# Performance work log

Hardware: AMD Instinct MI355X
Metric: run time of the kernel (lower is better)

## Reference

```python
import jax, jax.numpy as jnp
import numpy as np

HEADS = 8
GROUPS = 8
EPS = 1e-5

def setup_inputs() -> dict:
    key = jax.random.key(0)
    ks = jax.random.split(key, 12)
    B, C, S = 2, 256, 16
    x = jax.random.normal(ks[0], (B, C, S, S, S), dtype=jnp.float32)
    std = 1.0 / np.sqrt(C)
    def lin(k):
        kw, kb = jax.random.split(k)
        W = jax.random.uniform(kw, (C, C), jnp.float32, -std, std)
        b = jax.random.uniform(kb, (C,), jnp.float32, -std, std)
        return W, b
    Wq, bq = lin(ks[1])
    Wk, bk = lin(ks[2])
    Wv, bv = lin(ks[3])
    Wo, bo = lin(ks[4])
    gamma = jnp.ones((C,), jnp.float32)
    beta = jnp.zeros((C,), jnp.float32)
    return {"x": x, "gamma": gamma, "beta": beta, "Wq": Wq, "bq": bq,
            "Wk": Wk, "bk": bk, "Wv": Wv, "bv": bv, "Wo": Wo, "bo": bo}

def _group_norm(x, gamma, beta):
    B, C = x.shape[0], x.shape[1]
    xg = x.reshape(B, GROUPS, -1)  # [B, G, (C/G)*D*H*W]
    mu = xg.mean(axis=-1, keepdims=True)
    var = xg.var(axis=-1, keepdims=True)
    xg = (xg - mu) * jax.lax.rsqrt(var + EPS)
    xn = xg.reshape(x.shape)
    return xn * gamma[None, :, None, None, None] + beta[None, :, None, None, None]

def _conv1x1(x, W, b):
    # 1x1x1 Conv3d == channel-mixing linear: [B,C,D,H,W] x [O,C]
    return jnp.einsum('bcdhw,oc->bodhw', x, W) + b[None, :, None, None, None]

def reference(x, gamma, beta, Wq, bq, Wk, bk, Wv, bv, Wo, bo):
    B, C, D, H, W = x.shape
    hd = C // HEADS
    N = D * H * W
    xn = _group_norm(x, gamma, beta)
    Q = _conv1x1(xn, Wq, bq).reshape(B, HEADS, hd, N)
    K = _conv1x1(xn, Wk, bk).reshape(B, HEADS, hd, N)
    V = _conv1x1(xn, Wv, bv).reshape(B, HEADS, hd, N)
    scale = jnp.sqrt(jnp.asarray(hd, x.dtype))
    attn = jnp.einsum('bhdn,bhdm->bhnm', Q, K) / scale
    attn = jax.nn.softmax(attn, axis=-1)
    out = jnp.einsum('bhnm,bhdm->bhdn', attn, V).reshape(B, C, D, H, W)
    out = _conv1x1(out, Wo, bo)
    return x + out
```

## Files before the change

### kernel.cpp

```cpp
#include <hip/hip_runtime.h>

typedef unsigned short us;
typedef unsigned int uns;
typedef __attribute__((ext_vector_type(8))) short short8;
typedef __attribute__((ext_vector_type(4))) float floatx4;

__device__ __forceinline__ us f2b(float f) {
    union { float f; unsigned u; } x; x.f = f;
    unsigned r = x.u + 0x7fffu + ((x.u >> 16) & 1u);
    return (us)(r >> 16);
}
__device__ __forceinline__ uns fbits(float f) {
    union { float f; unsigned u; } x; x.f = f; return x.u;
}
__device__ __forceinline__ uns pk2(float hi, float lo) {
    return __builtin_amdgcn_perm(fbits(hi) + 0x8000u, fbits(lo) + 0x8000u, 0x07060302u);
}
__device__ __forceinline__ uns pk2t(float hi, float lo) {
    return __builtin_amdgcn_perm(fbits(hi), fbits(lo), 0x07060302u);
}
__device__ __forceinline__ float ex2(float x) {
    return __builtin_amdgcn_exp2f(x);
}

#define C_DIM 256
#define N_DIM 4096
#define CN (C_DIM * N_DIM)
#define CSC (0.17677669529663687f * 1.4426950408889634f)

__global__ __launch_bounds__(256) void k_part_prep(
        const float* __restrict__ x, float* __restrict__ part,
        const float* __restrict__ Wq, const float* __restrict__ Wk,
        const float* __restrict__ Wv, const float* __restrict__ Wo,
        const float* __restrict__ bq, const float* __restrict__ bk,
        const float* __restrict__ bv, const float* __restrict__ bo,
        us* __restrict__ Wb, float* __restrict__ bst) {
    const int t = threadIdx.x;
    if (blockIdx.y == 16) {
        const int xb = blockIdx.x;
#pragma unroll
        for (int e = 0; e < 4; ++e) {
            int id = e * 16384 + xb * 256 + t;
            Wb[id]          = f2b(Wq[id] * CSC);
            Wb[65536 + id]  = f2b(Wk[id]);
            Wb[131072 + id] = f2b(Wv[id]);
            Wb[196608 + id] = f2b(Wo[id]);
        }
        if (xb == 0) {
            bst[t]       = bq[t] * CSC;
            bst[256 + t] = bk[t];
            bst[512 + t] = bv[t];
            bst[768 + t] = bo[t];
        }
        return;
    }
    const int bg = blockIdx.y, sl = blockIdx.x;
    const float* base = x + (size_t)bg * 131072 + (size_t)sl * 2048 + t * 8;
    float4 a = *(const float4*)base;
    float4 b = *(const float4*)(base + 4);
    float s  = a.x + a.y + a.z + a.w + b.x + b.y + b.z + b.w;
    float ss = a.x*a.x + a.y*a.y + a.z*a.z + a.w*a.w
             + b.x*b.x + b.y*b.y + b.z*b.z + b.w*b.w;
    __shared__ float r1[256], r2[256];
    r1[t] = s; r2[t] = ss;
    __syncthreads();
    for (int off = 128; off > 0; off >>= 1) {
        if (t < off) { r1[t] += r1[t + off]; r2[t] += r2[t + off]; }
        __syncthreads();
    }
    if (t == 0) {
        part[(bg * 64 + sl) * 2]     = r1[0];
        part[(bg * 64 + sl) * 2 + 1] = r2[0];
    }
}

__global__ __launch_bounds__(256) void k_gn_normT(const float* __restrict__ x,
                                                  const float* __restrict__ gamma,
                                                  const float* __restrict__ beta,
                                                  const float* __restrict__ part,
                                                  us* __restrict__ XT) {
    const int t = threadIdx.x, g = blockIdx.y, z = blockIdx.z;
    const int bg = z * 8 + g;
    __shared__ float scs[32], offs[32], mv[2];
    if (t < 64) {
        float s  = part[(bg * 64 + t) * 2];
        float ss = part[(bg * 64 + t) * 2 + 1];
#pragma unroll
        for (int off = 1; off < 64; off <<= 1) {
            s  += __shfl_xor(s, off, 64);
            ss += __shfl_xor(ss, off, 64);
        }
        if (t == 0) {
            const float inv = 1.f / 131072.f;
            float mean = s * inv;
            float var  = ss * inv - mean * mean;
            mv[0] = mean; mv[1] = rsqrtf(var + 1e-5f);
        }
    }
    __syncthreads();
    if (t < 32) {
        float sc = mv[1] * gamma[g * 32 + t];
        scs[t]  = sc;
        offs[t] = beta[g * 32 + t] - mv[0] * sc;
    }
    __syncthreads();
    const int n = blockIdx.x * 256 + t;
    const float* xp = x + ((size_t)z * 256 + g * 32) * N_DIM + n;
    us* op = XT + ((size_t)z * N_DIM + n) * 256 + g * 32;
#pragma unroll
    for (int c8 = 0; c8 < 4; ++c8) {
        short8 o;
#pragma unroll
        for (int i = 0; i < 8; ++i) {
            int c = c8 * 8 + i;
            float v = xp[(size_t)c * N_DIM];
            o[i] = (short)f2b(v * scs[c] + offs[c]);
        }
        *(short8*)(op + c8 * 8) = o;
    }
}

__global__ __launch_bounds__(256) void k_qkv(const us* __restrict__ W,
                                             const float* __restrict__ bias,
                                             const us* __restrict__ XT,
                                             us* __restrict__ QT,
                                             us* __restrict__ KTg,
                                             us* __restrict__ Vb) {
    const int t = threadIdx.x;
    const int n0 = blockIdx.x * 64, m0 = blockIdx.y * 64, z = blockIdx.z;
    const int l = t & 63, w = t >> 6, l15 = l & 15, quad = l >> 4;
    const int wm = m0 + (w >> 1) * 32, wn = n0 + (w & 1) * 32;
    const us* Ap = W + (size_t)(wm + l15) * 256 + quad * 8;
    const us* Bp = XT + ((size_t)z * N_DIM + wn + l15) * 256 + quad * 8;

    floatx4 acc[2][2] = {};
#pragma unroll
    for (int k0 = 0; k0 < 256; k0 += 32) {
        short8 a0 = *(const short8*)(Ap + k0);
        short8 a1 = *(const short8*)(Ap + k0 + 16 * 256);
        short8 b0 = *(const short8*)(Bp + k0);
        short8 b1 = *(const short8*)(Bp + k0 + 16 * 256);
        acc[0][0] = __builtin_amdgcn_mfma_f32_16x16x32_bf16(a0, b0, acc[0][0], 0, 0, 0);
        acc[0][1] = __builtin_amdgcn_mfma_f32_16x16x32_bf16(a0, b1, acc[0][1], 0, 0, 0);
        acc[1][0] = __builtin_amdgcn_mfma_f32_16x16x32_bf16(a1, b0, acc[1][0], 0, 0, 0);
        acc[1][1] = __builtin_amdgcn_mfma_f32_16x16x32_bf16(a1, b1, acc[1][1], 0, 0, 0);
    }

    if (blockIdx.y < 8) {
        us* Dst = (blockIdx.y < 4) ? QT : KTg;
        const int h = (wm >> 5) & 7, bh = z * 8 + h;
#pragma unroll
        for (int mt = 0; mt < 2; ++mt) {
            const int d0 = mt * 16 + quad * 4;
            float b0v = bias[wm + mt * 16 + quad * 4 + 0];
            float b1v = bias[wm + mt * 16 + quad * 4 + 1];
            float b2v = bias[wm + mt * 16 + quad * 4 + 2];
            float b3v = bias[wm + mt * 16 + quad * 4 + 3];
#pragma unroll
            for (int nt = 0; nt < 2; ++nt) {
                int col = wn + nt * 16 + l15;
                uint2 pw;
                pw.x = pk2(acc[mt][nt][1] + b1v, acc[mt][nt][0] + b0v);
                pw.y = pk2(acc[mt][nt][3] + b3v, acc[mt][nt][2] + b2v);
                *(uint2*)(Dst + ((size_t)bh * N_DIM + col) * 32 + d0) = pw;
            }
        }
    } else {
#pragma unroll
        for (int mt = 0; mt < 2; ++mt)
#pragma unroll
            for (int nt = 0; nt < 2; ++nt)
#pragma unroll
                for (int r = 0; r < 4; ++r) {
                    int row = wm + mt * 16 + quad * 4 + r;
                    int col = wn + nt * 16 + l15;
                    Vb[((size_t)z * 256 + (row - 512)) * N_DIM + col] =
                        f2b(acc[mt][nt][r] + bias[row]);
                }
    }
}

__global__ __launch_bounds__(256, 2) void k_attn(const us* __restrict__ QT,
                                                 const us* __restrict__ KTg,
                                                 const us* __restrict__ Vb,
                                                 us* __restrict__ AOT) {
    __shared__ __attribute__((aligned(16))) us Kb[2][64 * 32];
    __shared__ __attribute__((aligned(16))) us Vl[2][32 * 64];
    __shared__ __attribute__((aligned(16))) us Pb[4][2][16 * 104];
    const int t = threadIdx.x;
    const int l = t & 63, w = t >> 6, l15 = l & 15, quad = l >> 4;
    const int bh = blockIdx.y, z = bh >> 3, h = bh & 7;
    const us* KTp = KTg + (size_t)bh * N_DIM * 32;
    const us* Vp  = Vb  + ((size_t)z * 256 + h * 32) * N_DIM;
    const int q0 = blockIdx.x * 128 + w * 32;

    short8 bq[2];
#pragma unroll
    for (int tl = 0; tl < 2; ++tl)
        bq[tl] = *(const short8*)(QT + ((size_t)bh * N_DIM + q0 + tl * 16 + l15) * 32 + quad * 8);
    short8 ones;
#pragma unroll
    for (int j = 0; j < 8; ++j) ones[j] = (short)0x3F80;

    floatx4 o1[2] = {}, o2[2] = {}, o3[2] = {};

    const int krow = w * 16 + (l >> 2), kslot = l & 3;
    const int kxs  = kslot ^ ((l >> 3) & 3);
    const us* kgs  = KTp + (size_t)krow * 32 + kslot * 8;
    us*       kds  = &Kb[0][0] + krow * 32 + kxs * 8;
    const int vrow = w * 8 + (l >> 3), vslot = l & 7;
    const int vxs  = vslot ^ ((l >> 3) & 7);
    const us* vgs  = Vp + (size_t)vrow * N_DIM + vslot * 8;
    us*       vds  = &Vl[0][0] + vrow * 64 + vxs * 8;

    const us* kfr = &Kb[0][0] + l15 * 32 + (quad ^ ((l15 >> 1) & 3)) * 8;
    const int vo1 = ( quad      ^ (l15 & 7)) * 8;
    const int vo2 = ((quad ^ 4) ^ (l15 & 7)) * 8;
    const us* vf1 = &Vl[0][0] +  l15       * 64 + vo1;
    const us* vf2 = &Vl[0][0] +  l15       * 64 + vo2;
    const us* vf3 = &Vl[0][0] + (16 + l15) * 64 + vo1;
    const us* vf4 = &Vl[0][0] + (16 + l15) * 64 + vo2;

    {
        int4 gk = *(const int4*)kgs;
        int4 gv = *(const int4*)vgs;
        *(int4*)kds = gk;
        *(int4*)vds = gv;
    }
    __syncthreads();
    int cur = 0;

    for (int m0 = 0; m0 < N_DIM; m0 += 64) {
        const int mnext = (m0 + 64) & (N_DIM - 1);
        int4 ngk = *(const int4*)(kgs + (size_t)mnext * 32);
        int4 ngv = *(const int4*)(vgs + mnext);

        const int bo = cur * 2048;
        short8 ak1 = *(const short8*)(kfr + bo);
        short8 ak2 = *(const short8*)(kfr + bo + 512);
        short8 ak3 = *(const short8*)(kfr + bo + 1024);
        short8 ak4 = *(const short8*)(kfr + bo + 1536);
        short8 a11 = *(const short8*)(vf1 + bo);
        short8 a12 = *(const short8*)(vf2 + bo);
        short8 a21 = *(const short8*)(vf3 + bo);
        short8 a22 = *(const short8*)(vf4 + bo);

#pragma unroll
        for (int tl = 0; tl < 2; ++tl) {
            floatx4 zz = {};
            floatx4 s1 = __builtin_amdgcn_mfma_f32_16x16x32_bf16(ak1, bq[tl], zz, 0, 0, 0);
            floatx4 s2 = __builtin_amdgcn_mfma_f32_16x16x32_bf16(ak2, bq[tl], zz, 0, 0, 0);
            floatx4 s3 = __builtin_amdgcn_mfma_f32_16x16x32_bf16(ak3, bq[tl], zz, 0, 0, 0);
            floatx4 s4 = __builtin_amdgcn_mfma_f32_16x16x32_bf16(ak4, bq[tl], zz, 0, 0, 0);
            us* pw = &Pb[w][tl][0] + l15 * 104 + quad * 4;
            uint2 p;
            p.x = pk2t(ex2(s1[1]), ex2(s1[0]));
            p.y = pk2t(ex2(s1[3]), ex2(s1[2]));
            *(uint2*)(pw) = p;
            p.x = pk2t(ex2(s2[1]), ex2(s2[0]));
            p.y = pk2t(ex2(s2[3]), ex2(s2[2]));
            *(uint2*)(pw + 16) = p;
            p.x = pk2t(ex2(s3[1]), ex2(s3[0]));
            p.y = pk2t(ex2(s3[3]), ex2(s3[2]));
            *(uint2*)(pw + 32) = p;
            p.x = pk2t(ex2(s4[1]), ex2(s4[0]));
            p.y = pk2t(ex2(s4[3]), ex2(s4[2]));
            *(uint2*)(pw + 48) = p;
        }

        asm volatile("s_waitcnt lgkmcnt(0)" ::: "memory");

#pragma unroll
        for (int tl = 0; tl < 2; ++tl) {
            const us* pr = &Pb[w][tl][0] + l15 * 104 + quad * 8;
            short8 pf1 = *(const short8*)(pr);
            short8 pf2 = *(const short8*)(pr + 32);
            o1[tl] = __builtin_amdgcn_mfma_f32_16x16x32_bf16(a11, pf1, o1[tl], 0, 0, 0);
            o2[tl] = __builtin_amdgcn_mfma_f32_16x16x32_bf16(a21, pf1, o2[tl], 0, 0, 0);
            o3[tl] = __builtin_amdgcn_mfma_f32_16x16x32_bf16(ones, pf1, o3[tl], 0, 0, 0);
            o1[tl] = __builtin_amdgcn_mfma_f32_16x16x32_bf16(a12, pf2, o1[tl], 0, 0, 0);
            o2[tl] = __builtin_amdgcn_mfma_f32_16x16x32_bf16(a22, pf2, o2[tl], 0, 0, 0);
            o3[tl] = __builtin_amdgcn_mfma_f32_16x16x32_bf16(ones, pf2, o3[tl], 0, 0, 0);
        }

        *(int4*)(kds + (cur ^ 1) * 2048) = ngk;
        *(int4*)(vds + (cur ^ 1) * 2048) = ngv;
        __syncthreads();
        cur ^= 1;
    }

#pragma unroll
    for (int tl = 0; tl < 2; ++tl) {
        const float inv = 1.f / o3[tl][0];
        const int q = q0 + tl * 16 + l15;
        us* op = AOT + ((size_t)z * N_DIM + q) * 256 + h * 32;
        uint2 lo, hi;
        lo.x = pk2(o1[tl][1] * inv, o1[tl][0] * inv);
        lo.y = pk2(o1[tl][3] * inv, o1[tl][2] * inv);
        hi.x = pk2(o2[tl][1] * inv, o2[tl][0] * inv);
        hi.y = pk2(o2[tl][3] * inv, o2[tl][2] * inv);
        *(uint2*)(op + quad * 4)      = lo;
        *(uint2*)(op + 16 + quad * 4) = hi;
    }
}

__global__ __launch_bounds__(256) void k_out(const us* __restrict__ W,
                                             const float* __restrict__ bias,
                                             const us* __restrict__ AOT,
                                             float* __restrict__ Out,
                                             const float* __restrict__ resid) {
    const int t = threadIdx.x;
    const int n0 = blockIdx.x * 64, m0 = blockIdx.y * 64, z = blockIdx.z;
    const int l = t & 63, w = t >> 6, l15 = l & 15, quad = l >> 4;
    const int wm = m0 + (w >> 1) * 32, wn = n0 + (w & 1) * 32;
    const us* Ap = W + (size_t)(wm + l15) * 256 + quad * 8;
    const us* Bp = AOT + ((size_t)z * N_DIM + wn + l15) * 256 + quad * 8;

    floatx4 acc[2][2] = {};
#pragma unroll
    for (int k0 = 0; k0 < 256; k0 += 32) {
        short8 a0 = *(const short8*)(Ap + k0);
        short8 a1 = *(const short8*)(Ap + k0 + 16 * 256);
        short8 b0 = *(const short8*)(Bp + k0);
        short8 b1 = *(const short8*)(Bp + k0 + 16 * 256);
        acc[0][0] = __builtin_amdgcn_mfma_f32_16x16x32_bf16(a0, b0, acc[0][0], 0, 0, 0);
        acc[0][1] = __builtin_amdgcn_mfma_f32_16x16x32_bf16(a0, b1, acc[0][1], 0, 0, 0);
        acc[1][0] = __builtin_amdgcn_mfma_f32_16x16x32_bf16(a1, b0, acc[1][0], 0, 0, 0);
        acc[1][1] = __builtin_amdgcn_mfma_f32_16x16x32_bf16(a1, b1, acc[1][1], 0, 0, 0);
    }

#pragma unroll
    for (int mt = 0; mt < 2; ++mt)
#pragma unroll
        for (int nt = 0; nt < 2; ++nt)
#pragma unroll
            for (int r = 0; r < 4; ++r) {
                int row = wm + mt * 16 + quad * 4 + r;
                int col = wn + nt * 16 + l15;
                size_t oidx = ((size_t)z * 256 + row) * N_DIM + col;
                Out[oidx] = acc[mt][nt][r] + bias[row] + resid[oidx];
            }
}

extern "C" void kernel_launch(void* const* d_in, const int* in_sizes, int n_in,
                              void* d_out, int out_size, void* d_ws, size_t ws_size,
                              hipStream_t stream) {
    (void)in_sizes; (void)n_in; (void)out_size; (void)ws_size;
    const float* x     = (const float*)d_in[0];
    const float* gamma = (const float*)d_in[1];
    const float* beta  = (const float*)d_in[2];
    const float* Wq = (const float*)d_in[3]; const float* bq = (const float*)d_in[4];
    const float* Wk = (const float*)d_in[5]; const float* bk = (const float*)d_in[6];
    const float* Wv = (const float*)d_in[7]; const float* bv = (const float*)d_in[8];
    const float* Wo = (const float*)d_in[9]; const float* bo = (const float*)d_in[10];

    float* part = (float*)d_ws;
    us*    Wb   = (us*)((char*)d_ws + 16384);
    float* bst  = (float*)((char*)d_ws + 16384 + 524288);
    us*    XT   = (us*)((char*)d_ws + 16384 + 524288 + 4096);
    us*    QT   = XT + 2 * CN;
    us*    AOT  = QT + 2 * CN;
    us*    Vb   = (us*)d_out;
    us*    KTg  = (us*)d_out + 2 * CN;

    k_part_prep<<<dim3(64, 17), dim3(256), 0, stream>>>(x, part, Wq, Wk, Wv, Wo,
                                                        bq, bk, bv, bo, Wb, bst);
    k_gn_normT<<<dim3(16, 8, 2), dim3(256), 0, stream>>>(x, gamma, beta, part, XT);
    k_qkv<<<dim3(64, 12, 2), dim3(256), 0, stream>>>(Wb, bst, XT, QT, KTg, Vb);
    k_attn<<<dim3(32, 16), dim3(256), 0, stream>>>(QT, KTg, Vb, AOT);
    k_out<<<dim3(64, 4, 2), dim3(256), 0, stream>>>(Wb + 196608, bst + 768, AOT,
                                                    (float*)d_out, x);
}
```

Measured before the change: 178.5 us.

## Use 32x32x16 MFMA in attention and keep P in registers via permlane swap

Switches the attention kernel from 16x16x32 to 32x32x16 bf16 MFMA tiles. The exponentiated scores are converted into B-operand fragments directly in registers with v_permlane32_swap, so the per-wave shared-memory P buffer, its store/reload and the lgkmcnt wait are gone. This removes LDS traffic and an explicit wait in the inner loop. In exchange it relies on the register layout of the 32x32 accumulator matching the required operand layout, and it uses larger accumulators that raise register pressure.

```diff
diff --git a/kernel.cpp b/kernel.cpp
--- a/kernel.cpp
+++ b/kernel.cpp
@@ -4,6 +4,8 @@
 typedef unsigned int uns;
 typedef __attribute__((ext_vector_type(8))) short short8;
 typedef __attribute__((ext_vector_type(4))) float floatx4;
+typedef __attribute__((ext_vector_type(16))) float floatx16;
+typedef __attribute__((ext_vector_type(4))) uns unsx4;
 
 __device__ __forceinline__ us f2b(float f) {
     union { float f; unsigned u; } x; x.f = f;
@@ -180,29 +182,50 @@
     }
 }
 
+__device__ __forceinline__ floatx16 mfma32(short8 a, short8 b, floatx16 c) {
+    return __builtin_amdgcn_mfma_f32_32x32x16_bf16(a, b, c, 0, 0, 0);
+}
+__device__ __forceinline__ void mkfrag(const floatx16& s, short8& p1, short8& p2) {
+    uns d0 = pk2t(ex2(s[1]),  ex2(s[0]));
+    uns d1 = pk2t(ex2(s[3]),  ex2(s[2]));
+    uns d2 = pk2t(ex2(s[5]),  ex2(s[4]));
+    uns d3 = pk2t(ex2(s[7]),  ex2(s[6]));
+    uns d4 = pk2t(ex2(s[9]),  ex2(s[8]));
+    uns d5 = pk2t(ex2(s[11]), ex2(s[10]));
+    uns d6 = pk2t(ex2(s[13]), ex2(s[12]));
+    uns d7 = pk2t(ex2(s[15]), ex2(s[14]));
+    asm volatile("v_permlane32_swap_b32 %0, %1" : "+v"(d0), "+v"(d2));
+    asm volatile("v_permlane32_swap_b32 %0, %1" : "+v"(d1), "+v"(d3));
+    asm volatile("v_permlane32_swap_b32 %0, %1" : "+v"(d4), "+v"(d6));
+    asm volatile("v_permlane32_swap_b32 %0, %1" : "+v"(d5), "+v"(d7));
+    unsx4 u1 = {d0, d1, d2, d3};
+    unsx4 u2 = {d4, d5, d6, d7};
+    p1 = __builtin_bit_cast(short8, u1);
+    p2 = __builtin_bit_cast(short8, u2);
+}
+
 __global__ __launch_bounds__(256, 2) void k_attn(const us* __restrict__ QT,
                                                  const us* __restrict__ KTg,
                                                  const us* __restrict__ Vb,
                                                  us* __restrict__ AOT) {
     __shared__ __attribute__((aligned(16))) us Kb[2][64 * 32];
     __shared__ __attribute__((aligned(16))) us Vl[2][32 * 64];
-    __shared__ __attribute__((aligned(16))) us Pb[4][2][16 * 104];
     const int t = threadIdx.x;
-    const int l = t & 63, w = t >> 6, l15 = l & 15, quad = l >> 4;
-    const int bh = blockIdx.y, z = bh >> 3, h = bh & 7;
+    const int l = t & 63, w = t >> 6, hf = l >> 5, k31 = l & 31;
+    const int bh = blockIdx.y, z = bh >> 3, hd = bh & 7;
     const us* KTp = KTg + (size_t)bh * N_DIM * 32;
-    const us* Vp  = Vb  + ((size_t)z * 256 + h * 32) * N_DIM;
+    const us* Vp  = Vb  + ((size_t)z * 256 + hd * 32) * N_DIM;
     const int q0 = blockIdx.x * 128 + w * 32;
 
-    short8 bq[2];
-#pragma unroll
-    for (int tl = 0; tl < 2; ++tl)
-        bq[tl] = *(const short8*)(QT + ((size_t)bh * N_DIM + q0 + tl * 16 + l15) * 32 + quad * 8);
+    const us* qb = QT + ((size_t)bh * N_DIM + q0 + k31) * 32 + hf * 8;
+    short8 bq1 = *(const short8*)qb;
+    short8 bq2 = *(const short8*)(qb + 16);
     short8 ones;
 #pragma unroll
     for (int j = 0; j < 8; ++j) ones[j] = (short)0x3F80;
 
-    floatx4 o1[2] = {}, o2[2] = {}, o3[2] = {};
+    floatx16 o  = (floatx16)0.0f;
+    floatx16 dn = (floatx16)0.0f;
 
     const int krow = w * 16 + (l >> 2), kslot = l & 3;
     const int kxs  = kslot ^ ((l >> 3) & 3);
@@ -213,13 +236,14 @@
     const us* vgs  = Vp + (size_t)vrow * N_DIM + vslot * 8;
     us*       vds  = &Vl[0][0] + vrow * 64 + vxs * 8;
 
-    const us* kfr = &Kb[0][0] + l15 * 32 + (quad ^ ((l15 >> 1) & 3)) * 8;
-    const int vo1 = ( quad      ^ (l15 & 7)) * 8;
-    const int vo2 = ((quad ^ 4) ^ (l15 & 7)) * 8;
-    const us* vf1 = &Vl[0][0] +  l15       * 64 + vo1;
-    const us* vf2 = &Vl[0][0] +  l15       * 64 + vo2;
-    const us* vf3 = &Vl[0][0] + (16 + l15) * 64 + vo1;
-    const us* vf4 = &Vl[0][0] + (16 + l15) * 64 + vo2;
+    const int kf = (k31 >> 1) & 3;
+    const us* ka0p = &Kb[0][0] + k31 * 32 + ((hf)     ^ kf) * 8;
+    const us* ka1p = &Kb[0][0] + k31 * 32 + ((2 + hf) ^ kf) * 8;
+    const int vf = k31 & 7;
+    const us* vp0 = &Vl[0][0] + k31 * 64 + ((0 + hf) ^ vf) * 8;
+    const us* vp1 = &Vl[0][0] + k31 * 64 + ((2 + hf) ^ vf) * 8;
+    const us* vp2 = &Vl[0][0] + k31 * 64 + ((4 + hf) ^ vf) * 8;
+    const us* vp3 = &Vl[0][0] + k31 * 64 + ((6 + hf) ^ vf) * 8;
 
     {
         int4 gk = *(const int4*)kgs;
@@ -236,52 +260,29 @@
         int4 ngv = *(const int4*)(vgs + mnext);
 
         const int bo = cur * 2048;
-        short8 ak1 = *(const short8*)(kfr + bo);
-        short8 ak2 = *(const short8*)(kfr + bo + 512);
-        short8 ak3 = *(const short8*)(kfr + bo + 1024);
-        short8 ak4 = *(const short8*)(kfr + bo + 1536);
-        short8 a11 = *(const short8*)(vf1 + bo);
-        short8 a12 = *(const short8*)(vf2 + bo);
-        short8 a21 = *(const short8*)(vf3 + bo);
-        short8 a22 = *(const short8*)(vf4 + bo);
-
-#pragma unroll
-        for (int tl = 0; tl < 2; ++tl) {
-            floatx4 zz = {};
-            floatx4 s1 = __builtin_amdgcn_mfma_f32_16x16x32_bf16(ak1, bq[tl], zz, 0, 0, 0);
-            floatx4 s2 = __builtin_amdgcn_mfma_f32_16x16x32_bf16(ak2, bq[tl], zz, 0, 0, 0);
-            floatx4 s3 = __builtin_amdgcn_mfma_f32_16x16x32_bf16(ak3, bq[tl], zz, 0, 0, 0);
-            floatx4 s4 = __builtin_amdgcn_mfma_f32_16x16x32_bf16(ak4, bq[tl], zz, 0, 0, 0);
-            us* pw = &Pb[w][tl][0] + l15 * 104 + quad * 4;
-            uint2 p;
-            p.x = pk2t(ex2(s1[1]), ex2(s1[0]));
-            p.y = pk2t(ex2(s1[3]), ex2(s1[2]));
-            *(uint2*)(pw) = p;
-            p.x = pk2t(ex2(s2[1]), ex2(s2[0]));
-            p.y = pk2t(ex2(s2[3]), ex2(s2[2]));
-            *(uint2*)(pw + 16) = p;
-            p.x = pk2t(ex2(s3[1]), ex2(s3[0]));
-            p.y = pk2t(ex2(s3[3]), ex2(s3[2]));
-            *(uint2*)(pw + 32) = p;
-            p.x = pk2t(ex2(s4[1]), ex2(s4[0]));
-            p.y = pk2t(ex2(s4[3]), ex2(s4[2]));
-            *(uint2*)(pw + 48) = p;
-        }
-
-        asm volatile("s_waitcnt lgkmcnt(0)" ::: "memory");
-
-#pragma unroll
-        for (int tl = 0; tl < 2; ++tl) {
-            const us* pr = &Pb[w][tl][0] + l15 * 104 + quad * 8;
-            short8 pf1 = *(const short8*)(pr);
-            short8 pf2 = *(const short8*)(pr + 32);
-            o1[tl] = __builtin_amdgcn_mfma_f32_16x16x32_bf16(a11, pf1, o1[tl], 0, 0, 0);
-            o2[tl] = __builtin_amdgcn_mfma_f32_16x16x32_bf16(a21, pf1, o2[tl], 0, 0, 0);
-            o3[tl] = __builtin_amdgcn_mfma_f32_16x16x32_bf16(ones, pf1, o3[tl], 0, 0, 0);
-            o1[tl] = __builtin_amdgcn_mfma_f32_16x16x32_bf16(a12, pf2, o1[tl], 0, 0, 0);
-            o2[tl] = __builtin_amdgcn_mfma_f32_16x16x32_bf16(a22, pf2, o2[tl], 0, 0, 0);
-            o3[tl] = __builtin_amdgcn_mfma_f32_16x16x32_bf16(ones, pf2, o3[tl], 0, 0, 0);
-        }
+        short8 ka0 = *(const short8*)(ka0p + bo);
+        short8 ka1 = *(const short8*)(ka1p + bo);
+        short8 kb0 = *(const short8*)(ka0p + bo + 1024);
+        short8 kb1 = *(const short8*)(ka1p + bo + 1024);
+        short8 v0  = *(const short8*)(vp0 + bo);
+        short8 v1  = *(const short8*)(vp1 + bo);
+        short8 v2  = *(const short8*)(vp2 + bo);
+        short8 v3  = *(const short8*)(vp3 + bo);
+
+        floatx16 s0 = (floatx16)0.0f, s1 = (floatx16)0.0f;
+        s0 = mfma32(ka0, bq1, s0);
+        s0 = mfma32(ka1, bq2, s0);
+        s1 = mfma32(kb0, bq1, s1);
+        s1 = mfma32(kb1, bq2, s1);
+
+        short8 p1, p2, p3, p4;
+        mkfrag(s0, p1, p2);
+        mkfrag(s1, p3, p4);
+
+        o  = mfma32(v0, p1, o);   dn = mfma32(ones, p1, dn);
+        o  = mfma32(v1, p2, o);   dn = mfma32(ones, p2, dn);
+        o  = mfma32(v2, p3, o);   dn = mfma32(ones, p3, dn);
+        o  = mfma32(v3, p4, o);   dn = mfma32(ones, p4, dn);
 
         *(int4*)(kds + (cur ^ 1) * 2048) = ngk;
         *(int4*)(vds + (cur ^ 1) * 2048) = ngv;
@@ -289,18 +290,15 @@
         cur ^= 1;
     }
 
-#pragma unroll
-    for (int tl = 0; tl < 2; ++tl) {
-        const float inv = 1.f / o3[tl][0];
-        const int q = q0 + tl * 16 + l15;
-        us* op = AOT + ((size_t)z * N_DIM + q) * 256 + h * 32;
-        uint2 lo, hi;
-        lo.x = pk2(o1[tl][1] * inv, o1[tl][0] * inv);
-        lo.y = pk2(o1[tl][3] * inv, o1[tl][2] * inv);
-        hi.x = pk2(o2[tl][1] * inv, o2[tl][0] * inv);
-        hi.y = pk2(o2[tl][3] * inv, o2[tl][2] * inv);
-        *(uint2*)(op + quad * 4)      = lo;
-        *(uint2*)(op + 16 + quad * 4) = hi;
+    const float inv = 1.f / dn[0];
+    const int q = q0 + k31;
+    us* op = AOT + ((size_t)z * N_DIM + q) * 256 + hd * 32 + hf * 4;
+#pragma unroll
+    for (int g = 0; g < 4; ++g) {
+        uint2 u;
+        u.x = pk2(o[4 * g + 1] * inv, o[4 * g + 0] * inv);
+        u.y = pk2(o[4 * g + 3] * inv, o[4 * g + 2] * inv);
+        *(uint2*)(op + 8 * g) = u;
     }
 }
 
```

After: 170.4 us. 4.6% less time.
